# Kernel optimization log

Hardware: AMD Instinct MI355X
Metric: run time of the kernel (lower is better)

The kernel has to match this reference:

```python
import jax, jax.numpy as jnp
import numpy as np

NUM_HEADS = 12
DIM_HEAD = 64
HIDDEN = 768


def _get_rel_pos(size, rel_pos):
    # q_size == k_size: relative coords in [0, 2*size-2]
    idx = jnp.arange(size)[:, None] - jnp.arange(size)[None, :] + (size - 1)
    return rel_pos[idx]  # (size, size, dim_head)


def setup_inputs() -> dict:
    key = jax.random.key(0)
    ks = jax.random.split(key, 5)
    B, H, W, C = 4, 32, 32, HIDDEN
    x = jax.random.normal(ks[0], (B, H, W, C), dtype=jnp.float32)
    w_qkv = jax.random.normal(ks[1], (C, 3 * NUM_HEADS * DIM_HEAD), dtype=jnp.float32) * (C ** -0.5)
    w_out = jax.random.normal(ks[2], (NUM_HEADS * DIM_HEAD, C), dtype=jnp.float32) * ((NUM_HEADS * DIM_HEAD) ** -0.5)
    b_out = jnp.zeros((C,), dtype=jnp.float32)
    rel_pos_h = jax.random.normal(ks[3], (2 * H - 1, DIM_HEAD), dtype=jnp.float32) * 0.02
    rel_pos_w = jax.random.normal(ks[4], (2 * W - 1, DIM_HEAD), dtype=jnp.float32) * 0.02
    return {"x": x, "w_qkv": w_qkv, "w_out": w_out, "b_out": b_out,
            "rel_pos_h": rel_pos_h, "rel_pos_w": rel_pos_w}


def reference(x, w_qkv, w_out, b_out, rel_pos_h, rel_pos_w):
    B, H, W, C = x.shape
    N = H * W
    nh, dh = NUM_HEADS, DIM_HEAD
    # qkv projection: (B, N, 3*nh*dh) split as (qkv, head, dim)
    qkv = x.reshape(B, N, C) @ w_qkv
    qkv = qkv.reshape(B, N, 3, nh, dh).transpose(2, 0, 3, 1, 4)  # (3, B, nh, N, dh)
    q, k, v = qkv[0], qkv[1], qkv[2]
    scale = dh ** -0.5
    attn = jnp.einsum('bhnd,bhmd->bhnm', q, k) * scale  # (B, nh, N, N)
    # decomposed relative positional bias (heads folded into batch)
    Rh = _get_rel_pos(H, rel_pos_h)  # (H, H, dh)
    Rw = _get_rel_pos(W, rel_pos_w)  # (W, W, dh)
    r_q = q.reshape(B * nh, H, W, dh)
    rel_h = jnp.einsum('bhwc,hkc->bhwk', r_q, Rh)  # (B*nh, H, W, H)
    rel_w = jnp.einsum('bhwc,wkc->bhwk', r_q, Rw)  # (B*nh, H, W, W)
    attn = (attn.reshape(B * nh, H, W, H, W)
            + rel_h[:, :, :, :, None]
            + rel_w[:, :, :, None, :]).reshape(B, nh, N, N)
    attn = jax.nn.softmax(attn, axis=-1)
    out = jnp.einsum('bhnm,bhmd->bhnd', attn, v)  # (B, nh, N, dh)
    out = out.transpose(0, 2, 1, 3).reshape(B, N, nh * dh)
    return out @ w_out + b_out  # (B, N, hidden)
```

## Files before the change

### kernel.cpp

```cpp
#include <hip/hip_runtime.h>
#include <cstdint>

#define DEV __device__ __forceinline__

typedef __bf16  bf16x8 __attribute__((ext_vector_type(8)));
typedef short   s16x8  __attribute__((ext_vector_type(8)));
typedef float   f32x4  __attribute__((ext_vector_type(4)));

#define QSCALE 0.18033688011112042f
#define MOFF   17.312340490667560f

DEV unsigned short f2bf(float f){
  union { float f; unsigned u; } v; v.f = f;
  unsigned r = v.u + 0x7fffu + ((v.u >> 16) & 1u);
  return (unsigned short)(r >> 16);
}

DEV unsigned pk2(float lo, float hi){
  unsigned a = __builtin_bit_cast(unsigned, lo) + 0x8000u;
  unsigned b = __builtin_bit_cast(unsigned, hi) + 0x8000u;
  return __builtin_amdgcn_perm(b, a, 0x07060302);
}

DEV void gl2lds16(const void* g, void* l){
  __builtin_amdgcn_global_load_lds((__attribute__((address_space(1))) void*)(void*)(g),
                                   (__attribute__((address_space(3))) void*)(l), 16, 0, 0);
}

DEV f32x4 mfma16(bf16x8 a, bf16x8 b, f32x4 c){
  return __builtin_amdgcn_mfma_f32_16x16x32_bf16(a, b, c, 0, 0, 0);
}

__global__ __launch_bounds__(256) void prep_kernel(const float* __restrict__ x,
                                                   short* __restrict__ xb,
                                                   const float* __restrict__ rph,
                                                   const float* __restrict__ rpw,
                                                   short* __restrict__ rphb,
                                                   short* __restrict__ rpwb,
                                                   const float* __restrict__ w_qkv,
                                                   short* __restrict__ wqT,
                                                   const float* __restrict__ w_out,
                                                   short* __restrict__ woT){
  __shared__ float tb[32][33];
  int b = blockIdx.x;
  if (b < 1536){
    int i = b * 256 + threadIdx.x;
    const float4* in4 = (const float4*)x;
    float4 f0 = in4[i*2], f1 = in4[i*2+1];
    s16x8 o;
    o[0]=(short)f2bf(f0.x); o[1]=(short)f2bf(f0.y); o[2]=(short)f2bf(f0.z); o[3]=(short)f2bf(f0.w);
    o[4]=(short)f2bf(f1.x); o[5]=(short)f2bf(f1.y); o[6]=(short)f2bf(f1.z); o[7]=(short)f2bf(f1.w);
    *(s16x8*)(xb + i*8) = o;
  } else if (b == 1536){
    int t = threadIdx.x;
    for (int j = 0; j < 16; j++){
      int idx = t*16 + j;
      if (idx < 4032){
        rphb[idx] = (short)f2bf(rph[idx] * 8.f);
        rpwb[idx] = (short)f2bf(rpw[idx] * 8.f);
      }
    }
  } else {
    const float* in; short* out; int R, C, bx, by;
    if (b < 3265){ int t = b - 1537; in = w_qkv; out = wqT; R = 768; C = 2304; bx = t % 72; by = t / 72; }
    else         { int t = b - 3265; in = w_out; out = woT; R = 768; C = 768;  bx = t % 24; by = t / 24; }
    int tx = threadIdx.x & 31, ty = threadIdx.x >> 5;
    int c0 = bx * 32, r0 = by * 32;
    for (int i = 0; i < 4; i++)
      tb[ty + i*8][tx] = in[(r0 + ty + i*8)*C + c0 + tx];
    __syncthreads();
    for (int i = 0; i < 4; i++)
      out[(c0 + ty + i*8)*R + r0 + tx] = (short)f2bf(tb[tx][ty + i*8]);
  }
}

__global__ __launch_bounds__(256) void qkv_gemm_kernel(const short* __restrict__ xb,
                                                       const short* __restrict__ wqT,
                                                       short* __restrict__ qb,
                                                       short* __restrict__ kb,
                                                       short* __restrict__ vtb){
  __shared__ __align__(16) short As[128*64];
  __shared__ __align__(16) short Bs[96*64];
  const int tid = threadIdx.x, lane = tid & 63, wv = tid >> 6;
  const int quad = lane >> 4, mi = lane & 15;
  const int flat = blockIdx.x + (blockIdx.y << 5);
  const int xcd = flat & 7, s = flat >> 3;
  const int bx = (xcd & 3)*8 + (s & 7);
  const int by = (xcd >> 2)*12 + (s >> 3);
  const int m0 = bx * 128, n0 = by * 96;
  const int wrow = wv >> 1, wcol = wv & 1;
  const int srow = lane >> 3, scs = lane & 7;
  const int sc = scs ^ (srow & 7);
  f32x4 acc[4][3] = {};
  for (int k0 = 0; k0 < 768; k0 += 64){
    __syncthreads();
    for (int i = 0; i < 4; i++){
      int rbase = i*32 + wv*8;
      int row = rbase + srow;
      gl2lds16(xb + (m0+row)*768 + k0 + sc*8, As + rbase*64 + lane*8);
    }
    for (int i = 0; i < 3; i++){
      int rbase = i*32 + wv*8;
      int row = rbase + srow;
      gl2lds16(wqT + (n0+row)*768 + k0 + sc*8, Bs + rbase*64 + lane*8);
    }
    __syncthreads();
    bf16x8 a[2][4], b[2][3];
#pragma unroll
    for (int kk = 0; kk < 2; kk++){
      int ccs = ((quad + kk*4) ^ (mi & 7)) * 8;
      for (int mt = 0; mt < 4; mt++) a[kk][mt] = *(const bf16x8*)(As + (wrow*64 + mt*16 + mi)*64 + ccs);
      for (int nt = 0; nt < 3; nt++) b[kk][nt] = *(const bf16x8*)(Bs + (wcol*48 + nt*16 + mi)*64 + ccs);
    }
#pragma unroll
    for (int kk = 0; kk < 2; kk++)
      for (int mt = 0; mt < 4; mt++)
        for (int nt = 0; nt < 3; nt++)
          acc[mt][nt] = mfma16(a[kk][mt], b[kk][nt], acc[mt][nt]);
  }
  const int which = n0 / 768;
  if (which == 2){
    for (int nt = 0; nt < 3; nt++){
      int j = n0 + wcol*48 + nt*16 + mi;
      int rem = j % 768;
      int head = rem >> 6, d = rem & 63;
      for (int mt = 0; mt < 4; mt++)
        for (int r = 0; r < 4; r++){
          int m = m0 + wrow*64 + mt*16 + quad*4 + r;
          int bh = (m >> 10)*12 + head;
          vtb[((bh*64 + d) << 10) + (m & 1023)] = (short)f2bf(acc[mt][nt][r]);
        }
    }
  } else {
    const float qs = (which == 0) ? QSCALE : 1.0f;
    short* dst = (which == 0) ? qb : kb;
    for (int nt = 0; nt < 3; nt++){
      int j = n0 + wcol*48 + nt*16 + mi;
      int rem = j % 768;
      int head = rem >> 6, d = rem & 63;
      for (int mt = 0; mt < 4; mt++)
        for (int r = 0; r < 4; r++){
          int m = m0 + wrow*64 + mt*16 + quad*4 + r;
          int bh = (m >> 10)*12 + head;
          dst[((bh << 10) + (m & 1023))*64 + d] = (short)f2bf(acc[mt][nt][r] * qs);
        }
    }
  }
}

__global__ __launch_bounds__(256) void relw_kernel(const short* __restrict__ qb,
                                                   const short* __restrict__ rpwb,
                                                   float* __restrict__ relW){
  int wv = threadIdx.x >> 6, lane = threadIdx.x & 63;
  int bid2 = blockIdx.x*4 + wv;
  int quad = lane >> 4, mi = lane & 15;
  f32x4 acc[2] = {};
  int w = bid2 / 96, rt = bid2 % 96;
  int rg = rt*16 + mi, bh = rg >> 5, h = rg & 31;
  const short* qr = qb + (bh*1024 + h*32 + w)*64;
  bf16x8 a0 = *(const bf16x8*)(qr + quad*8);
  bf16x8 a1 = *(const bf16x8*)(qr + 32 + quad*8);
  for (int nt = 0; nt < 2; nt++){
    int kw = nt*16 + mi;
    const short* rr = rpwb + (w - kw + 31)*64;
    bf16x8 b0 = *(const bf16x8*)(rr + quad*8);
    bf16x8 b1 = *(const bf16x8*)(rr + 32 + quad*8);
    acc[nt] = mfma16(a0, b0, acc[nt]);
    acc[nt] = mfma16(a1, b1, acc[nt]);
  }
  for (int nt = 0; nt < 2; nt++)
    for (int r = 0; r < 4; r++){
      int rowg = rt*16 + quad*4 + r;
      relW[(rowg*32 + w)*32 + nt*16 + mi] = acc[nt][r];
    }
}

__global__ __launch_bounds__(256, 3) void flash_kernel(const short* __restrict__ qb,
                                                       const short* __restrict__ kb,
                                                       const short* __restrict__ vtb,
                                                       const float* __restrict__ relW,
                                                       const short* __restrict__ rphb,
                                                       short* __restrict__ ao){
  __shared__ __align__(16) short Qt[64*64];
  __shared__ __align__(16) short Kt[64*64];
  __shared__ __align__(16) short Vt[64*64];
  __shared__ __align__(16) short Pt[64*64];
  __shared__ __align__(16) float rHs[32*64];
  __shared__ __align__(16) float rWs[64*32];
  const int tid = threadIdx.x, lane = tid & 63, wv = tid >> 6;
  const int quad = lane >> 4, mi = lane & 15;
  const int flat = blockIdx.x + (blockIdx.y << 4);
  const int nw = (flat & 7)*96 + (flat >> 3);
  const int bh = nw >> 4, n0 = (nw & 15) << 6;
  const int sw0 = (quad ^ (mi & 7)) * 8;
  const int sw1 = ((quad + 4) ^ (mi & 7)) * 8;
  const int qrow = wv*16 + mi;
  const int srow = lane >> 3;

  const short* kg = kb  + bh*1024*64;
  const short* vg = vtb + bh*64*1024;

  {
    const short* qg  = qb   + (bh*1024 + n0)*64;
    const float* rwg = relW + (bh*1024 + n0)*32;
    for (int i = 0; i < 2; i++){
      int slab = wv*2 + i, rbase = slab*8;
      int row = rbase + srow;
      int c = (lane & 7) ^ (row & 7);
      gl2lds16(qg + row*64 + c*8, Qt + rbase*64 + lane*8);
      gl2lds16(rwg + slab*256 + lane*4, rWs + slab*256 + lane*4);
    }
  }
  __syncthreads();

  bf16x8 qf0 = *(const bf16x8*)(Qt + qrow*64 + sw0);
  bf16x8 qf1 = *(const bf16x8*)(Qt + qrow*64 + sw1);
  float rw[2][4];
#pragma unroll
  for (int s = 0; s < 2; s++)
    for (int r = 0; r < 4; r++)
      rw[s][r] = rWs[qrow*32 + s*16 + quad*4 + r];

  {
    int h = (n0 + wv*16) >> 5;
    const short* rp = rphb + (h + 31 - mi)*64;
#pragma unroll
    for (int khb = 0; khb < 2; khb++){
      const short* rk = rp - khb*1024;
      bf16x8 a0 = *(const bf16x8*)(rk + quad*8);
      bf16x8 a1 = *(const bf16x8*)(rk + 32 + quad*8);
      f32x4 c = {};
      c = mfma16(a0, qf0, c);
      c = mfma16(a1, qf1, c);
      for (int r = 0; r < 4; r++)
        rHs[(khb*16 + quad*4 + r)*64 + wv*16 + mi] = c[r] - MOFF;
    }
  }

  f32x4 O[4] = {};
  float l_ = 0.f;

  for (int step = 0; step < 16; step++){
    {
      const short* kt = kg + step*64*64;
      for (int i = 0; i < 2; i++){
        int slab = wv*2 + i, rbase = slab*8;
        int row = rbase + srow;
        int c = (lane & 7) ^ (row & 7);
        gl2lds16(kt + row*64 + c*8, Kt + rbase*64 + lane*8);
        gl2lds16(vg + row*1024 + step*64 + c*8, Vt + rbase*64 + lane*8);
      }
    }
    __syncthreads();

    f32x4 S[4];
#pragma unroll
    for (int nt = 0; nt < 4; nt++){
      bf16x8 kf0 = *(const bf16x8*)(Kt + (nt*16 + mi)*64 + sw0);
      bf16x8 kf1 = *(const bf16x8*)(Kt + (nt*16 + mi)*64 + sw1);
      f32x4 c = {};
      c = mfma16(kf0, qf0, c);
      c = mfma16(kf1, qf1, c);
      S[nt] = c;
    }
    float kh0 = rHs[(2*step)*64 + qrow];
    float kh1 = rHs[(2*step + 1)*64 + qrow];
#pragma unroll
    for (int nt = 0; nt < 4; nt++){
      float kh = (nt & 2) ? kh1 : kh0;
      for (int r = 0; r < 4; r++){
        float p = __builtin_amdgcn_exp2f(S[nt][r] + kh + rw[nt & 1][r]);
        S[nt][r] = p;
        l_ += p;
      }
    }
#pragma unroll
    for (int nt = 0; nt < 4; nt++){
      unsigned u0 = pk2(S[nt][0], S[nt][1]);
      unsigned u1 = pk2(S[nt][2], S[nt][3]);
      int chunk = (2*nt + (quad >> 1)) ^ (mi & 7);
      uint2 uu; uu.x = u0; uu.y = u1;
      *(uint2*)(Pt + qrow*64 + chunk*8 + (quad & 1)*4) = uu;
    }
    bf16x8 p0 = *(const bf16x8*)(Pt + qrow*64 + sw0);
    bf16x8 p1 = *(const bf16x8*)(Pt + qrow*64 + sw1);
#pragma unroll
    for (int t = 0; t < 4; t++){
      bf16x8 v0 = *(const bf16x8*)(Vt + (t*16 + mi)*64 + sw0);
      bf16x8 v1 = *(const bf16x8*)(Vt + (t*16 + mi)*64 + sw1);
      O[t] = mfma16(p0, v0, O[t]);
      O[t] = mfma16(p1, v1, O[t]);
    }
    __syncthreads();
  }

  l_ += __shfl_xor(l_, 16, 64);
  l_ += __shfl_xor(l_, 32, 64);
  float inv[4];
#pragma unroll
  for (int r = 0; r < 4; r++) inv[r] = 1.f / __shfl(l_, quad*4 + r, 64);
  int b_ = bh / 12, head = bh % 12;
#pragma unroll
  for (int t = 0; t < 4; t++)
    for (int r = 0; r < 4; r++){
      int n = n0 + wv*16 + quad*4 + r;
      ao[(b_*1024 + n)*768 + head*64 + t*16 + mi] = (short)f2bf(O[t][r] * inv[r]);
    }
}

__global__ __launch_bounds__(256) void proj_kernel(const short* __restrict__ ao,
                                                   const short* __restrict__ woT,
                                                   const float* __restrict__ bias,
                                                   float* __restrict__ out){
  __shared__ __align__(16) short As[64*64];
  __shared__ __align__(16) short Bs[96*64];
  const int tid = threadIdx.x, lane = tid & 63, wv = tid >> 6;
  const int quad = lane >> 4, mi = lane & 15;
  const int m0 = blockIdx.x * 64, n0 = blockIdx.y * 96;
  const int wrow = wv >> 1, wcol = wv & 1;
  const int srow = lane >> 3, sc = (lane & 7) ^ (srow & 7);
  f32x4 acc[2][3] = {};
  for (int k0 = 0; k0 < 768; k0 += 64){
    __syncthreads();
    for (int i = 0; i < 2; i++){
      int rbase = i*32 + wv*8, row = rbase + srow;
      gl2lds16(ao + (m0+row)*768 + k0 + sc*8, As + rbase*64 + lane*8);
    }
    for (int i = 0; i < 3; i++){
      int rbase = i*32 + wv*8, row = rbase + srow;
      gl2lds16(woT + (n0+row)*768 + k0 + sc*8, Bs + rbase*64 + lane*8);
    }
    __syncthreads();
    bf16x8 a[2][2], b[2][3];
#pragma unroll
    for (int kk = 0; kk < 2; kk++){
      int ccs = ((quad + kk*4) ^ (mi & 7)) * 8;
      for (int mt = 0; mt < 2; mt++) a[kk][mt] = *(const bf16x8*)(As + (wrow*32 + mt*16 + mi)*64 + ccs);
      for (int nt = 0; nt < 3; nt++) b[kk][nt] = *(const bf16x8*)(Bs + (wcol*48 + nt*16 + mi)*64 + ccs);
    }
#pragma unroll
    for (int kk = 0; kk < 2; kk++)
      for (int mt = 0; mt < 2; mt++)
        for (int nt = 0; nt < 3; nt++)
          acc[mt][nt] = mfma16(a[kk][mt], b[kk][nt], acc[mt][nt]);
  }
  for (int nt = 0; nt < 3; nt++){
    int j = n0 + wcol*48 + nt*16 + mi;
    float bj = bias[j];
    for (int mt = 0; mt < 2; mt++)
      for (int r = 0; r < 4; r++){
        int m = m0 + wrow*32 + mt*16 + quad*4 + r;
        out[m*768 + j] = acc[mt][nt][r] + bj;
      }
  }
}

extern "C" void kernel_launch(void* const* d_in, const int* in_sizes, int n_in,
                              void* d_out, int out_size, void* d_ws, size_t ws_size,
                              hipStream_t stream){
  const float* x     = (const float*)d_in[0];
  const float* w_qkv = (const float*)d_in[1];
  const float* w_out = (const float*)d_in[2];
  const float* b_out = (const float*)d_in[3];
  const float* rph   = (const float*)d_in[4];
  const float* rpw   = (const float*)d_in[5];
  float* out = (float*)d_out;
  char* ws = (char*)d_ws;
  short* xb    = (short*)(ws + 0);
  short* wqT   = (short*)(ws + 6291456);
  short* woT   = (short*)(ws + 9830400);
  short* qb    = (short*)(ws + 11010048);
  short* kb    = (short*)(ws + 17301504);
  short* vtb   = (short*)(ws + 29884416);
  float* relW  = (float*)(ws + 42467328);
  short* rphb  = (short*)(ws + 48758784);
  short* rpwb  = (short*)(ws + 48775168);
  short* ao    = xb;

  prep_kernel<<<3841, 256, 0, stream>>>(x, xb, rph, rpw, rphb, rpwb, w_qkv, wqT, w_out, woT);
  qkv_gemm_kernel<<<dim3(32, 24), 256, 0, stream>>>(xb, wqT, qb, kb, vtb);
  relw_kernel<<<768, 256, 0, stream>>>(qb, rpwb, relW);
  flash_kernel<<<dim3(16, 48), 256, 0, stream>>>(qb, kb, vtb, relW, rphb, ao);
  proj_kernel<<<dim3(64, 8), 256, 0, stream>>>(ao, woT, b_out, out);
}
```

Before: 151.6 us.

## Fuse relative-width bias computation into flash attention kernel

Removes the separate relw_kernel and the fp32 relW buffer. Each flash block now computes q·rel_pos_w for all 64 relative offsets with MFMA into LDS, aliased onto the Q tile buffer, then gathers the needed 32 entries per row. The rel_pos_w bf16 table is padded with zeros to 64 rows. This drops one launch and the global write and read of relW, at the cost of extra MFMAs and one more barrier in the flash prologue.

```diff
diff --git a/kernel.cpp b/kernel.cpp
--- a/kernel.cpp
+++ b/kernel.cpp
@@ -58,6 +58,8 @@
       if (idx < 4032){
         rphb[idx] = (short)f2bf(rph[idx] * 8.f);
         rpwb[idx] = (short)f2bf(rpw[idx] * 8.f);
+      } else if (idx < 4096){
+        rpwb[idx] = 0;
       }
     }
   } else {
@@ -148,45 +150,19 @@
   }
 }
 
-__global__ __launch_bounds__(256) void relw_kernel(const short* __restrict__ qb,
-                                                   const short* __restrict__ rpwb,
-                                                   float* __restrict__ relW){
-  int wv = threadIdx.x >> 6, lane = threadIdx.x & 63;
-  int bid2 = blockIdx.x*4 + wv;
-  int quad = lane >> 4, mi = lane & 15;
-  f32x4 acc[2] = {};
-  int w = bid2 / 96, rt = bid2 % 96;
-  int rg = rt*16 + mi, bh = rg >> 5, h = rg & 31;
-  const short* qr = qb + (bh*1024 + h*32 + w)*64;
-  bf16x8 a0 = *(const bf16x8*)(qr + quad*8);
-  bf16x8 a1 = *(const bf16x8*)(qr + 32 + quad*8);
-  for (int nt = 0; nt < 2; nt++){
-    int kw = nt*16 + mi;
-    const short* rr = rpwb + (w - kw + 31)*64;
-    bf16x8 b0 = *(const bf16x8*)(rr + quad*8);
-    bf16x8 b1 = *(const bf16x8*)(rr + 32 + quad*8);
-    acc[nt] = mfma16(a0, b0, acc[nt]);
-    acc[nt] = mfma16(a1, b1, acc[nt]);
-  }
-  for (int nt = 0; nt < 2; nt++)
-    for (int r = 0; r < 4; r++){
-      int rowg = rt*16 + quad*4 + r;
-      relW[(rowg*32 + w)*32 + nt*16 + mi] = acc[nt][r];
-    }
-}
-
 __global__ __launch_bounds__(256, 3) void flash_kernel(const short* __restrict__ qb,
                                                        const short* __restrict__ kb,
                                                        const short* __restrict__ vtb,
-                                                       const float* __restrict__ relW,
                                                        const short* __restrict__ rphb,
+                                                       const short* __restrict__ rpwb,
                                                        short* __restrict__ ao){
-  __shared__ __align__(16) short Qt[64*64];
+  __shared__ __align__(16) char QE[16384];
   __shared__ __align__(16) short Kt[64*64];
   __shared__ __align__(16) short Vt[64*64];
   __shared__ __align__(16) short Pt[64*64];
   __shared__ __align__(16) float rHs[32*64];
-  __shared__ __align__(16) float rWs[64*32];
+  short* Qt = (short*)QE;
+  float* Es = (float*)QE;
   const int tid = threadIdx.x, lane = tid & 63, wv = tid >> 6;
   const int quad = lane >> 4, mi = lane & 15;
   const int flat = blockIdx.x + (blockIdx.y << 4);
@@ -201,25 +177,18 @@
   const short* vg = vtb + bh*64*1024;
 
   {
-    const short* qg  = qb   + (bh*1024 + n0)*64;
-    const float* rwg = relW + (bh*1024 + n0)*32;
+    const short* qg = qb + (bh*1024 + n0)*64;
     for (int i = 0; i < 2; i++){
       int slab = wv*2 + i, rbase = slab*8;
       int row = rbase + srow;
       int c = (lane & 7) ^ (row & 7);
       gl2lds16(qg + row*64 + c*8, Qt + rbase*64 + lane*8);
-      gl2lds16(rwg + slab*256 + lane*4, rWs + slab*256 + lane*4);
     }
   }
   __syncthreads();
 
   bf16x8 qf0 = *(const bf16x8*)(Qt + qrow*64 + sw0);
   bf16x8 qf1 = *(const bf16x8*)(Qt + qrow*64 + sw1);
-  float rw[2][4];
-#pragma unroll
-  for (int s = 0; s < 2; s++)
-    for (int r = 0; r < 4; r++)
-      rw[s][r] = rWs[qrow*32 + s*16 + quad*4 + r];
 
   {
     int h = (n0 + wv*16) >> 5;
@@ -235,6 +204,28 @@
       for (int r = 0; r < 4; r++)
         rHs[(khb*16 + quad*4 + r)*64 + wv*16 + mi] = c[r] - MOFF;
     }
+  }
+
+  __syncthreads();
+
+#pragma unroll
+  for (int jt = 0; jt < 4; jt++){
+    const short* rr = rpwb + (jt*16 + mi)*64;
+    bf16x8 a0 = *(const bf16x8*)(rr + quad*8);
+    bf16x8 a1 = *(const bf16x8*)(rr + 32 + quad*8);
+    f32x4 c = {};
+    c = mfma16(a0, qf0, c);
+    c = mfma16(a1, qf1, c);
+    for (int r = 0; r < 4; r++)
+      Es[(jt*16 + quad*4 + r)*64 + qrow] = c[r];
+  }
+  float rw[2][4];
+  {
+    int w31 = (qrow & 31) + 31;
+#pragma unroll
+    for (int s = 0; s < 2; s++)
+      for (int r = 0; r < 4; r++)
+        rw[s][r] = Es[(w31 - (s*16 + quad*4 + r))*64 + qrow];
   }
 
   f32x4 O[4] = {};
@@ -372,14 +363,12 @@
   short* qb    = (short*)(ws + 11010048);
   short* kb    = (short*)(ws + 17301504);
   short* vtb   = (short*)(ws + 29884416);
-  float* relW  = (float*)(ws + 42467328);
   short* rphb  = (short*)(ws + 48758784);
   short* rpwb  = (short*)(ws + 48775168);
   short* ao    = xb;
 
   prep_kernel<<<3841, 256, 0, stream>>>(x, xb, rph, rpw, rphb, rpwb, w_qkv, wqT, w_out, woT);
   qkv_gemm_kernel<<<dim3(32, 24), 256, 0, stream>>>(xb, wqT, qb, kb, vtb);
-  relw_kernel<<<768, 256, 0, stream>>>(qb, rpwb, relW);
-  flash_kernel<<<dim3(16, 48), 256, 0, stream>>>(qb, kb, vtb, relW, rphb, ao);
+  flash_kernel<<<dim3(16, 48), 256, 0, stream>>>(qb, kb, vtb, rphb, rpwb, ao);
   proj_kernel<<<dim3(64, 8), 256, 0, stream>>>(ao, woT, b_out, out);
 }
```

Measured after the change: 153.1 us. About the same (+1.0%).
